# Optimization experiments

Measured on AMD Instinct MI355X. Metric: run time of the kernel, lower is better.

Reference implementation:

```python
import jax, jax.numpy as jnp
import numpy as np

D_MODEL = 1024
N_HEADS = 16
D_Q = D_MODEL // N_HEADS
NEG = float(-2**32 + 1)


def setup_inputs() -> dict:
    key = jax.random.key(0)
    ks = jax.random.split(key, 8)
    B, L = 8, 1024
    q = jax.random.normal(ks[0], (B, L, D_MODEL), dtype=jnp.float32)
    k = jax.random.normal(ks[1], (B, L, D_MODEL), dtype=jnp.float32)
    # causal subsequent mask: 1 above the diagonal (positions to be masked)
    subseq_mask = jnp.broadcast_to(
        jnp.triu(jnp.ones((L, L), dtype=jnp.int32), k=1), (B, L, L))
    s = 1.0 / np.sqrt(D_MODEL)
    Wq = jax.random.normal(ks[2], (D_MODEL, D_MODEL), dtype=jnp.float32) * s
    Wk = jax.random.normal(ks[3], (D_MODEL, D_MODEL), dtype=jnp.float32) * s
    Wv = jax.random.normal(ks[4], (D_MODEL, D_MODEL), dtype=jnp.float32) * s
    bq = jax.random.normal(ks[5], (D_MODEL,), dtype=jnp.float32) * 0.01
    bk = jax.random.normal(ks[6], (D_MODEL,), dtype=jnp.float32) * 0.01
    bv = jax.random.normal(ks[7], (D_MODEL,), dtype=jnp.float32) * 0.01
    return {"q": q, "k": k, "subseq_mask": subseq_mask,
            "Wq": Wq, "bq": bq, "Wk": Wk, "bk": bk, "Wv": Wv, "bv": bv}


def reference(q, k, subseq_mask, Wq, bq, Wk, bk, Wv, bv):
    B, Lq, _ = q.shape
    Lk = k.shape[1]
    residual = q
    # projections; heads laid out as (H, B, L, d_q) matching torch permute(2,0,1,3)
    qp = (q @ Wq + bq).reshape(B, Lq, N_HEADS, D_Q).transpose(2, 0, 1, 3)
    kp = (k @ Wk + bk).reshape(B, Lk, N_HEADS, D_Q).transpose(2, 0, 1, 3)
    vp = (k @ Wv + bv).reshape(B, Lk, N_HEADS, D_Q).transpose(2, 0, 1, 3)
    # scaled scores: (H, B, Lq, Lk)
    scores = jnp.einsum('hbqd,hbkd->hbqk', qp, kp) / np.sqrt(D_Q)
    # key mask from PROJECTED k (faithful to source)
    key_masks = jnp.sign(jnp.abs(jnp.sum(kp, -1)))          # (H, B, Lk)
    scores = jnp.where(key_masks[:, :, None, :] == 0, NEG, scores)
    # subsequence (causal) mask, replicated over heads
    scores = jnp.where(subseq_mask[None, :, :, :] == 1, NEG, scores)
    attn = jax.nn.softmax(scores, axis=-1)
    # post-softmax query mask from PROJECTED q (faithful to source)
    query_masks = jnp.sign(jnp.abs(jnp.sum(qp, -1)))        # (H, B, Lq)
    attn = attn * query_masks[:, :, :, None]
    # dropout is identity in eval/reference mode
    out = jnp.einsum('hbqk,hbkd->hbqd', attn, vp)           # (H, B, Lq, d_q)
    out = out.transpose(1, 2, 0, 3).reshape(B, Lq, N_HEADS * D_Q)
    return out + residual
```

## Files before the change

### kernel.cpp

```cpp
#include <hip/hip_runtime.h>
#include <cstdint>
#include <cstddef>

#define DM 1024
#define NH 16
#define DQ 64
#define NB 8
#define LSEQ 1024

typedef __attribute__((ext_vector_type(8))) short short8;
typedef __attribute__((ext_vector_type(4))) float floatx4;

__device__ __forceinline__ unsigned short f2bf(float f) {
  union { float f; unsigned u; } v; v.f = f;
  unsigned r = v.u + 0x7FFFu + ((v.u >> 16) & 1u);
  return (unsigned short)(r >> 16);
}
__device__ __forceinline__ float bf2f(unsigned short u) {
  union { unsigned u; float f; } v; v.u = ((unsigned)u) << 16;
  return v.f;
}

__device__ __forceinline__ void async_load16(const void* g, void* l) {
  __builtin_amdgcn_global_load_lds(
      (const __attribute__((address_space(1))) unsigned int*)g,
      (__attribute__((address_space(3))) unsigned int*)l, 16, 0, 0);
}

__global__ void convert_qk(const float* __restrict__ q, const float* __restrict__ k,
                           unsigned short* __restrict__ qb, unsigned short* __restrict__ kb) {
  size_t i = ((size_t)blockIdx.x * 256 + threadIdx.x) * 4;
  float4 a = *(const float4*)&q[i];
  ushort4 r;
  r.x = f2bf(a.x); r.y = f2bf(a.y); r.z = f2bf(a.z); r.w = f2bf(a.w);
  *(ushort4*)&qb[i] = r;
  float4 b = *(const float4*)&k[i];
  ushort4 s;
  s.x = f2bf(b.x); s.y = f2bf(b.y); s.z = f2bf(b.z); s.w = f2bf(b.w);
  *(ushort4*)&kb[i] = s;
}

__global__ void transpose_w(const float* __restrict__ Wq, const float* __restrict__ Wk,
                            const float* __restrict__ Wv, unsigned short* __restrict__ Wt) {
  int z = blockIdx.z;
  const float* W = (z == 0) ? Wq : (z == 1) ? Wk : Wv;
  __shared__ float tile[32][33];
  int n0 = blockIdx.x * 32, k0 = blockIdx.y * 32;
  int tx = threadIdx.x;
  for (int j = threadIdx.y; j < 32; j += 8)
    tile[j][tx] = W[(size_t)(k0 + j) * DM + n0 + tx];
  __syncthreads();
  unsigned short* o = Wt + (size_t)z * DM * DM;
  for (int j = threadIdx.y; j < 32; j += 8)
    o[(size_t)(n0 + j) * DM + k0 + tx] = f2bf(tile[tx][j]);
}

__global__ __launch_bounds__(256, 4) void gemm_proj(
    const unsigned short* __restrict__ qb, const unsigned short* __restrict__ kb,
    const unsigned short* __restrict__ Wt,
    const float* __restrict__ bq, const float* __restrict__ bk, const float* __restrict__ bv,
    const float* __restrict__ ,
    unsigned short* __restrict__ Pq, unsigned short* __restrict__ Pk,
    unsigned short* __restrict__ Pvt,
    float* __restrict__ qmask, float* __restrict__ kmask) {
  const int z = blockIdx.z;
  const unsigned short* A = (z == 0) ? qb : kb;
  const unsigned short* Bt = Wt + (size_t)z * DM * DM;
  const float* bias = (z == 0) ? bq : (z == 1) ? bk : bv;

  __shared__ unsigned short smem[16384];
  unsigned short* As = smem;
  unsigned short* Bs = smem + 8192;

  const int tid = threadIdx.x;
  const int lane = tid & 63;
  const int wave = tid >> 6;
  const int l16 = lane & 15, quad = lane >> 4;
  const int wm = wave & 1, wn = wave >> 1;
  const int rowBase = blockIdx.x * 128;
  const int colBase = blockIdx.y * 128;

  floatx4 acc[4][4];
  const floatx4 zf = {0.f, 0.f, 0.f, 0.f};
#pragma unroll
  for (int i = 0; i < 4; i++)
#pragma unroll
    for (int j = 0; j < 4; j++) acc[i][j] = zf;

  const int srl = lane >> 3;
  const int sl7 = lane & 7;

  for (int kt = 0; kt < DM; kt += 64) {
#pragma unroll
    for (int cc = wave; cc < 16; cc += 4) {
      const int rl = cc * 8 + srl;
      const int ck = (sl7 ^ (rl & 7)) * 8;
      async_load16(A + (size_t)(rowBase + rl) * DM + kt + ck, &As[cc * 512]);
      async_load16(Bt + (size_t)(colBase + rl) * DM + kt + ck, &Bs[cc * 512]);
    }
    __syncthreads();

#pragma unroll
    for (int c = 0; c < 2; c++) {
      const int chnk = ((c << 2) + quad) ^ (l16 & 7);
      short8 af[4], bfr[4];
#pragma unroll
      for (int i = 0; i < 4; i++)
        af[i] = *(const short8*)&As[(wm * 64 + i * 16 + l16) * 64 + chnk * 8];
#pragma unroll
      for (int j = 0; j < 4; j++)
        bfr[j] = *(const short8*)&Bs[(wn * 64 + j * 16 + l16) * 64 + chnk * 8];
#pragma unroll
      for (int i = 0; i < 4; i++)
#pragma unroll
        for (int j = 0; j < 4; j++)
          acc[i][j] = __builtin_amdgcn_mfma_f32_16x16x32_bf16(af[i], bfr[j], acc[i][j], 0, 0, 0);
    }
    __syncthreads();
  }

#pragma unroll
  for (int j = 0; j < 4; j++) {
    const float bj = bias[colBase + wn * 64 + j * 16 + l16];
#pragma unroll
    for (int i = 0; i < 4; i++)
#pragma unroll
      for (int r = 0; r < 4; r++) acc[i][j][r] += bj;
  }

  if (z < 2) {
    float* mask = (z == 0) ? qmask : kmask;
    const int h = (colBase >> 6) + wn;
#pragma unroll
    for (int i = 0; i < 4; i++)
#pragma unroll
      for (int r = 0; r < 4; r++) {
        float rs = acc[i][0][r] + acc[i][1][r] + acc[i][2][r] + acc[i][3][r];
        rs += __shfl_xor(rs, 1);
        rs += __shfl_xor(rs, 2);
        rs += __shfl_xor(rs, 4);
        rs += __shfl_xor(rs, 8);
        if (l16 == 0) {
          const int row = rowBase + wm * 64 + i * 16 + quad * 4 + r;
          mask[((size_t)((row >> 10) * NH + h)) * LSEQ + (row & 1023)] = (rs != 0.f) ? 1.f : 0.f;
        }
      }
    unsigned short* P = (z == 0) ? Pq : Pk;
    const int bb2 = rowBase >> 10;
    const int l0 = (rowBase & 1023) + wm * 64;
    const size_t pbase = ((size_t)(bb2 * NH + h) * LSEQ + l0) * DQ;
    unsigned short* lds = smem + wave * 2304;
#pragma unroll
    for (int pass = 0; pass < 2; ++pass) {
#pragma unroll
      for (int ii = 0; ii < 2; ++ii) {
        const int i = pass * 2 + ii;
#pragma unroll
        for (int j = 0; j < 4; ++j)
#pragma unroll
          for (int r = 0; r < 4; ++r)
            lds[(ii * 16 + quad * 4 + r) * 72 + j * 16 + l16] = f2bf(acc[i][j][r]);
      }
      asm volatile("s_waitcnt lgkmcnt(0)" ::: "memory");
#pragma unroll
      for (int ll = 0; ll < 4; ++ll) {
        const int c = ll * 8 + (lane >> 3);
        const int seg = lane & 7;
        int4 v = *(const int4*)&lds[c * 72 + seg * 8];
        *(int4*)&P[pbase + (size_t)(pass * 32 + c) * DQ + seg * 8] = v;
      }
      if (pass == 0) asm volatile("s_waitcnt lgkmcnt(0)" ::: "memory");
    }
  } else {
    const int b = rowBase >> 10;
    const int l0r = rowBase & 1023;
#pragma unroll
    for (int j = 0; j < 4; j++) {
      __syncthreads();
#pragma unroll
      for (int i = 0; i < 4; i++) {
        ushort4 v;
        v.x = f2bf(acc[i][j][0]); v.y = f2bf(acc[i][j][1]);
        v.z = f2bf(acc[i][j][2]); v.w = f2bf(acc[i][j][3]);
        *(ushort4*)&smem[(wn * 16 + l16) * 136 + wm * 64 + i * 16 + quad * 4] = v;
      }
      __syncthreads();
      const int c = tid >> 3, seg = tid & 7;
      const int col = colBase + (c >> 4) * 64 + j * 16 + (c & 15);
      const int hh = col >> 6, d = col & 63;
      int4 t0 = *(const int4*)&smem[c * 136 + seg * 16];
      int4 t1 = *(const int4*)&smem[c * 136 + seg * 16 + 8];
      const size_t g = ((size_t)((b * NH + hh) * DQ + d)) * LSEQ + l0r + seg * 16;
      *(int4*)&Pvt[g] = t0;
      *(int4*)&Pvt[g + 8] = t1;
    }
  }
}

__global__ __launch_bounds__(256, 4) void attn_kernel(
    const unsigned short* __restrict__ Q, const unsigned short* __restrict__ K,
    const unsigned short* __restrict__ Vt,
    const float* __restrict__ kmask, const float* __restrict__ qmask,
    const float* __restrict__ qin, float* __restrict__ out) {
  const int bh = blockIdx.x;
  const int qblk = 7 - blockIdx.y;
  const int b = bh >> 4, h = bh & 15;
  const size_t base = (size_t)bh * LSEQ * DQ;

  const int tid = threadIdx.x;
  const int lane = tid & 63;
  const int wave = tid >> 6;
  const int l16 = lane & 15, quad = lane >> 4;
  const int qw = qblk * 128 + wave * 32;

  __shared__ unsigned short Ks[2 * 4096];
  __shared__ unsigned short Vs[2 * 4096];
  __shared__ unsigned short Ps[4][2304];

  short8 qf[2][2];
#pragma unroll
  for (int sub = 0; sub < 2; sub++)
#pragma unroll
    for (int c = 0; c < 2; c++) {
      short8 t = *(const short8*)&Q[base + (size_t)(qw + sub * 16 + l16) * DQ + c * 32 + quad * 8];
#pragma unroll
      for (int e = 0; e < 8; e++) t[e] = (short)f2bf(bf2f((unsigned short)t[e]) * 0.125f);
      qf[sub][c] = t;
    }

  const floatx4 zf = {0.f, 0.f, 0.f, 0.f};
  floatx4 o[2][4];
#pragma unroll
  for (int sub = 0; sub < 2; sub++)
#pragma unroll
    for (int jj = 0; jj < 4; jj++) o[sub][jj] = zf;
  float l_p[2][4] = {{0.f, 0.f, 0.f, 0.f}, {0.f, 0.f, 0.f, 0.f}};

  const int swz = (quad ^ (l16 & 7)) * 8;
  const int swz2 = ((quad + 4) ^ (l16 & 7)) * 8;
  const int vswz = (quad ^ (l16 >> 1)) * 8;
  const int vswz2 = ((quad + 4) ^ (l16 >> 1)) * 8;

  const int srl = (lane >> 3);
  const int ktiles = (qblk + 1) * 2;
  const int tmax = 2 * qblk + (wave >> 1);

  {
#pragma unroll
    for (int cc = wave; cc < 8; cc += 4) {
      const int rl = cc * 8 + srl;
      const int ck = ((lane & 7) ^ (rl & 7)) * 8;
      async_load16(&K[base + (size_t)rl * DQ + ck], &Ks[cc * 512]);
      const int cv = ((lane & 7) ^ ((rl >> 1) & 7)) * 8;
      async_load16(&Vt[base + (size_t)rl * LSEQ + cv], &Vs[cc * 512]);
    }
  }
  __syncthreads();

  for (int t = 0; t < ktiles; t++) {
    const int cur = t & 1;
    const int kt = t * 64;
    const bool live = (t <= tmax);

    float km[4];
    if (live) {
#pragma unroll
      for (int ct = 0; ct < 4; ct++) km[ct] = kmask[(size_t)bh * LSEQ + kt + ct * 16 + l16];
    }

    if (t + 1 < ktiles) {
      const int nkt = kt + 64;
      const int nb = (cur ^ 1) * 4096;
#pragma unroll
      for (int cc = wave; cc < 8; cc += 4) {
        const int rl = cc * 8 + srl;
        const int ck = ((lane & 7) ^ (rl & 7)) * 8;
        async_load16(&K[base + (size_t)(nkt + rl) * DQ + ck], &Ks[nb + cc * 512]);
        const int cv = ((lane & 7) ^ ((rl >> 1) & 7)) * 8;
        async_load16(&Vt[base + (size_t)rl * LSEQ + nkt + cv], &Vs[nb + cc * 512]);
      }
    }

    if (live) {
      const unsigned short* Kb = &Ks[cur * 4096];
      const unsigned short* Vb = &Vs[cur * 4096];
      const bool diag = (t == tmax);

#pragma unroll
      for (int sub = 0; sub < 2; sub++) {
        floatx4 s[4];
#pragma unroll
        for (int ct = 0; ct < 4; ct++) {
          const int kr = (ct * 16 + l16) * 64;
          const short8 kf0 = *(const short8*)&Kb[kr + swz];
          const short8 kf1 = *(const short8*)&Kb[kr + swz2];
          floatx4 sv = zf;
          sv = __builtin_amdgcn_mfma_f32_16x16x32_bf16(qf[sub][0], kf0, sv, 0, 0, 0);
          sv = __builtin_amdgcn_mfma_f32_16x16x32_bf16(qf[sub][1], kf1, sv, 0, 0, 0);
          s[ct] = sv;
        }
        const int row0 = qw + sub * 16 + quad * 4;
        unsigned short* pw = &Ps[wave][(sub * 16 + quad * 4) * 72];
        if (diag) {
#pragma unroll
          for (int ct = 0; ct < 4; ct++) {
            const int col = kt + ct * 16 + l16;
#pragma unroll
            for (int r = 0; r < 4; r++) {
              float e = __expf(s[ct][r]) * km[ct];
              e = (col <= row0 + r) ? e : 0.f;
              l_p[sub][r] += e;
              pw[r * 72 + ct * 16 + l16] = f2bf(e);
            }
          }
        } else {
#pragma unroll
          for (int ct = 0; ct < 4; ct++) {
#pragma unroll
            for (int r = 0; r < 4; r++) {
              float e = __expf(s[ct][r]) * km[ct];
              l_p[sub][r] += e;
              pw[r * 72 + ct * 16 + l16] = f2bf(e);
            }
          }
        }
      }
      asm volatile("s_waitcnt lgkmcnt(0)" ::: "memory");

      short8 pf[2][2];
#pragma unroll
      for (int sub = 0; sub < 2; sub++) {
        pf[sub][0] = *(const short8*)&Ps[wave][(sub * 16 + l16) * 72 + quad * 8];
        pf[sub][1] = *(const short8*)&Ps[wave][(sub * 16 + l16) * 72 + 32 + quad * 8];
      }
#pragma unroll
      for (int jj = 0; jj < 4; jj++) {
        const int vr = (jj * 16 + l16) * 64;
        const short8 vf0 = *(const short8*)&Vb[vr + vswz];
        const short8 vf1 = *(const short8*)&Vb[vr + vswz2];
#pragma unroll
        for (int sub = 0; sub < 2; sub++) {
          o[sub][jj] = __builtin_amdgcn_mfma_f32_16x16x32_bf16(pf[sub][0], vf0, o[sub][jj], 0, 0, 0);
          o[sub][jj] = __builtin_amdgcn_mfma_f32_16x16x32_bf16(pf[sub][1], vf1, o[sub][jj], 0, 0, 0);
        }
      }
    }
    __syncthreads();
  }

  const int hd = h * DQ;
#pragma unroll
  for (int sub = 0; sub < 2; sub++)
#pragma unroll
    for (int r = 0; r < 4; r++) {
      float lv = l_p[sub][r];
      lv += __shfl_xor(lv, 1);
      lv += __shfl_xor(lv, 2);
      lv += __shfl_xor(lv, 4);
      lv += __shfl_xor(lv, 8);
      const int row = qw + sub * 16 + quad * 4 + r;
      const float inv = qmask[(size_t)bh * LSEQ + row] / lv;
#pragma unroll
      for (int jj = 0; jj < 4; jj++) {
        const size_t oi = ((size_t)(b * LSEQ + row)) * DM + hd + jj * 16 + l16;
        out[oi] = o[sub][jj][r] * inv + qin[oi];
      }
    }
}

extern "C" void kernel_launch(void* const* d_in, const int* in_sizes, int n_in,
                              void* d_out, int out_size, void* d_ws, size_t ws_size,
                              hipStream_t stream) {
  const float* q = (const float*)d_in[0];
  const float* k = (const float*)d_in[1];
  const float* Wq = (const float*)d_in[3];
  const float* bq = (const float*)d_in[4];
  const float* Wk = (const float*)d_in[5];
  const float* bk = (const float*)d_in[6];
  const float* Wv = (const float*)d_in[7];
  const float* bv = (const float*)d_in[8];
  float* out = (float*)d_out;

  char* w = (char*)d_ws;
  unsigned short* qb = (unsigned short*)(w + 0);
  unsigned short* kb = (unsigned short*)(w + 16777216);
  unsigned short* Wt = (unsigned short*)(w + 33554432);
  unsigned short* Pq = (unsigned short*)(w + 39845888);
  unsigned short* Pk = (unsigned short*)(w + 56623104);
  unsigned short* Pvt = (unsigned short*)(w + 73400320);
  float* qmask = (float*)(w + 90177536);
  float* kmask = (float*)(w + 90701824);

  convert_qk<<<8192, 256, 0, stream>>>(q, k, qb, kb);
  transpose_w<<<dim3(32, 32, 3), dim3(32, 8), 0, stream>>>(Wq, Wk, Wv, Wt);
  gemm_proj<<<dim3(64, 8, 3), 256, 0, stream>>>(qb, kb, Wt, bq, bk, bv, nullptr,
                                                Pq, Pk, Pvt, qmask, kmask);
  attn_kernel<<<dim3(128, 8), 256, 0, stream>>>(Pq, Pk, Pvt, kmask, qmask, q, out);
}
```

Before: 253.8 us.

## Load K/V fragments directly from global memory and fold query scale into projection

```diff
diff --git a/kernel.cpp b/kernel.cpp
--- a/kernel.cpp
+++ b/kernel.cpp
@@ -146,6 +146,7 @@
         }
       }
     unsigned short* P = (z == 0) ? Pq : Pk;
+    const float pscale = (z == 0) ? 0.125f : 1.0f;
     const int bb2 = rowBase >> 10;
     const int l0 = (rowBase & 1023) + wm * 64;
     const size_t pbase = ((size_t)(bb2 * NH + h) * LSEQ + l0) * DQ;
@@ -159,7 +160,7 @@
         for (int j = 0; j < 4; ++j)
 #pragma unroll
           for (int r = 0; r < 4; ++r)
-            lds[(ii * 16 + quad * 4 + r) * 72 + j * 16 + l16] = f2bf(acc[i][j][r]);
+            lds[(ii * 16 + quad * 4 + r) * 72 + j * 16 + l16] = f2bf(acc[i][j][r] * pscale);
       }
       asm volatile("s_waitcnt lgkmcnt(0)" ::: "memory");
 #pragma unroll
@@ -213,20 +214,14 @@
   const int l16 = lane & 15, quad = lane >> 4;
   const int qw = qblk * 128 + wave * 32;
 
-  __shared__ unsigned short Ks[2 * 4096];
-  __shared__ unsigned short Vs[2 * 4096];
   __shared__ unsigned short Ps[4][2304];
 
   short8 qf[2][2];
 #pragma unroll
   for (int sub = 0; sub < 2; sub++)
 #pragma unroll
-    for (int c = 0; c < 2; c++) {
-      short8 t = *(const short8*)&Q[base + (size_t)(qw + sub * 16 + l16) * DQ + c * 32 + quad * 8];
-#pragma unroll
-      for (int e = 0; e < 8; e++) t[e] = (short)f2bf(bf2f((unsigned short)t[e]) * 0.125f);
-      qf[sub][c] = t;
-    }
+    for (int c = 0; c < 2; c++)
+      qf[sub][c] = *(const short8*)&Q[base + (size_t)(qw + sub * 16 + l16) * DQ + c * 32 + quad * 8];
 
   const floatx4 zf = {0.f, 0.f, 0.f, 0.f};
   floatx4 o[2][4];
@@ -236,116 +231,85 @@
     for (int jj = 0; jj < 4; jj++) o[sub][jj] = zf;
   float l_p[2][4] = {{0.f, 0.f, 0.f, 0.f}, {0.f, 0.f, 0.f, 0.f}};
 
-  const int swz = (quad ^ (l16 & 7)) * 8;
-  const int swz2 = ((quad + 4) ^ (l16 & 7)) * 8;
-  const int vswz = (quad ^ (l16 >> 1)) * 8;
-  const int vswz2 = ((quad + 4) ^ (l16 >> 1)) * 8;
-
-  const int srl = (lane >> 3);
-  const int ktiles = (qblk + 1) * 2;
   const int tmax = 2 * qblk + (wave >> 1);
 
-  {
-#pragma unroll
-    for (int cc = wave; cc < 8; cc += 4) {
-      const int rl = cc * 8 + srl;
-      const int ck = ((lane & 7) ^ (rl & 7)) * 8;
-      async_load16(&K[base + (size_t)rl * DQ + ck], &Ks[cc * 512]);
-      const int cv = ((lane & 7) ^ ((rl >> 1) & 7)) * 8;
-      async_load16(&Vt[base + (size_t)rl * LSEQ + cv], &Vs[cc * 512]);
-    }
-  }
-  __syncthreads();
-
-  for (int t = 0; t < ktiles; t++) {
-    const int cur = t & 1;
+  for (int t = 0; t <= tmax; t++) {
     const int kt = t * 64;
-    const bool live = (t <= tmax);
+    const bool diag = (t == tmax);
 
     float km[4];
-    if (live) {
-#pragma unroll
-      for (int ct = 0; ct < 4; ct++) km[ct] = kmask[(size_t)bh * LSEQ + kt + ct * 16 + l16];
-    }
-
-    if (t + 1 < ktiles) {
-      const int nkt = kt + 64;
-      const int nb = (cur ^ 1) * 4096;
-#pragma unroll
-      for (int cc = wave; cc < 8; cc += 4) {
-        const int rl = cc * 8 + srl;
-        const int ck = ((lane & 7) ^ (rl & 7)) * 8;
-        async_load16(&K[base + (size_t)(nkt + rl) * DQ + ck], &Ks[nb + cc * 512]);
-        const int cv = ((lane & 7) ^ ((rl >> 1) & 7)) * 8;
-        async_load16(&Vt[base + (size_t)rl * LSEQ + nkt + cv], &Vs[nb + cc * 512]);
-      }
-    }
-
-    if (live) {
-      const unsigned short* Kb = &Ks[cur * 4096];
-      const unsigned short* Vb = &Vs[cur * 4096];
-      const bool diag = (t == tmax);
-
-#pragma unroll
-      for (int sub = 0; sub < 2; sub++) {
-        floatx4 s[4];
+#pragma unroll
+    for (int ct = 0; ct < 4; ct++) km[ct] = kmask[(size_t)bh * LSEQ + kt + ct * 16 + l16];
+
+    short8 kf[4][2];
+#pragma unroll
+    for (int ct = 0; ct < 4; ct++) {
+      const unsigned short* kp = &K[base + (size_t)(kt + ct * 16 + l16) * DQ + quad * 8];
+      kf[ct][0] = *(const short8*)kp;
+      kf[ct][1] = *(const short8*)(kp + 32);
+    }
+
+#pragma unroll
+    for (int sub = 0; sub < 2; sub++) {
+      floatx4 s[4];
+#pragma unroll
+      for (int ct = 0; ct < 4; ct++) {
+        floatx4 sv = zf;
+        sv = __builtin_amdgcn_mfma_f32_16x16x32_bf16(qf[sub][0], kf[ct][0], sv, 0, 0, 0);
+        sv = __builtin_amdgcn_mfma_f32_16x16x32_bf16(qf[sub][1], kf[ct][1], sv, 0, 0, 0);
+        s[ct] = sv;
+      }
+      const int row0 = qw + sub * 16 + quad * 4;
+      unsigned short* pw = &Ps[wave][(sub * 16 + quad * 4) * 72];
+      if (diag) {
 #pragma unroll
         for (int ct = 0; ct < 4; ct++) {
-          const int kr = (ct * 16 + l16) * 64;
-          const short8 kf0 = *(const short8*)&Kb[kr + swz];
-          const short8 kf1 = *(const short8*)&Kb[kr + swz2];
-          floatx4 sv = zf;
-          sv = __builtin_amdgcn_mfma_f32_16x16x32_bf16(qf[sub][0], kf0, sv, 0, 0, 0);
-          sv = __builtin_amdgcn_mfma_f32_16x16x32_bf16(qf[sub][1], kf1, sv, 0, 0, 0);
-          s[ct] = sv;
-        }
-        const int row0 = qw + sub * 16 + quad * 4;
-        unsigned short* pw = &Ps[wave][(sub * 16 + quad * 4) * 72];
-        if (diag) {
-#pragma unroll
-          for (int ct = 0; ct < 4; ct++) {
-            const int col = kt + ct * 16 + l16;
-#pragma unroll
-            for (int r = 0; r < 4; r++) {
-              float e = __expf(s[ct][r]) * km[ct];
-              e = (col <= row0 + r) ? e : 0.f;
-              l_p[sub][r] += e;
-              pw[r * 72 + ct * 16 + l16] = f2bf(e);
-            }
-          }
-        } else {
-#pragma unroll
-          for (int ct = 0; ct < 4; ct++) {
-#pragma unroll
-            for (int r = 0; r < 4; r++) {
-              float e = __expf(s[ct][r]) * km[ct];
-              l_p[sub][r] += e;
-              pw[r * 72 + ct * 16 + l16] = f2bf(e);
-            }
+          const int col = kt + ct * 16 + l16;
+#pragma unroll
+          for (int r = 0; r < 4; r++) {
+            float e = __expf(s[ct][r]) * km[ct];
+            e = (col <= row0 + r) ? e : 0.f;
+            l_p[sub][r] += e;
+            pw[r * 72 + ct * 16 + l16] = f2bf(e);
           }
         }
-      }
-      asm volatile("s_waitcnt lgkmcnt(0)" ::: "memory");
-
-      short8 pf[2][2];
+      } else {
+#pragma unroll
+        for (int ct = 0; ct < 4; ct++) {
+#pragma unroll
+          for (int r = 0; r < 4; r++) {
+            float e = __expf(s[ct][r]) * km[ct];
+            l_p[sub][r] += e;
+            pw[r * 72 + ct * 16 + l16] = f2bf(e);
+          }
+        }
+      }
+    }
+
+    short8 vf[4][2];
+#pragma unroll
+    for (int jj = 0; jj < 4; jj++) {
+      const unsigned short* vp = &Vt[base + (size_t)(jj * 16 + l16) * LSEQ + kt + quad * 8];
+      vf[jj][0] = *(const short8*)vp;
+      vf[jj][1] = *(const short8*)(vp + 32);
+    }
+    asm volatile("s_waitcnt lgkmcnt(0)" ::: "memory");
+
+    short8 pf[2][2];
+#pragma unroll
+    for (int sub = 0; sub < 2; sub++) {
+      pf[sub][0] = *(const short8*)&Ps[wave][(sub * 16 + l16) * 72 + quad * 8];
+      pf[sub][1] = *(const short8*)&Ps[wave][(sub * 16 + l16) * 72 + 32 + quad * 8];
+    }
+#pragma unroll
+    for (int jj = 0; jj < 4; jj++) {
 #pragma unroll
       for (int sub = 0; sub < 2; sub++) {
-        pf[sub][0] = *(const short8*)&Ps[wave][(sub * 16 + l16) * 72 + quad * 8];
-        pf[sub][1] = *(const short8*)&Ps[wave][(sub * 16 + l16) * 72 + 32 + quad * 8];
-      }
-#pragma unroll
-      for (int jj = 0; jj < 4; jj++) {
-        const int vr = (jj * 16 + l16) * 64;
-        const short8 vf0 = *(const short8*)&Vb[vr + vswz];
-        const short8 vf1 = *(const short8*)&Vb[vr + vswz2];
-#pragma unroll
-        for (int sub = 0; sub < 2; sub++) {
-          o[sub][jj] = __builtin_amdgcn_mfma_f32_16x16x32_bf16(pf[sub][0], vf0, o[sub][jj], 0, 0, 0);
-          o[sub][jj] = __builtin_amdgcn_mfma_f32_16x16x32_bf16(pf[sub][1], vf1, o[sub][jj], 0, 0, 0);
-        }
-      }
-    }
-    __syncthreads();
+        o[sub][jj] = __builtin_amdgcn_mfma_f32_16x16x32_bf16(pf[sub][0], vf[jj][0], o[sub][jj], 0, 0, 0);
+        o[sub][jj] = __builtin_amdgcn_mfma_f32_16x16x32_bf16(pf[sub][1], vf[jj][1], o[sub][jj], 0, 0, 0);
+      }
+    }
+    asm volatile("s_waitcnt lgkmcnt(0)" ::: "memory");
   }
 
   const int hd = h * DQ;
```

After: 290.6 us. 1.14x slower.
